# Kernel optimization log

Measured on AMD Instinct MI355X. Metric: run time of the kernel, lower is better.

## Reference

```python
import jax, jax.numpy as jnp
import numpy as np

N_NODES = 207
N_EDGES = 1722
N_SLOTS = 288  # 288 / resolution with resolution = 1


def setup_inputs() -> dict:
    key = jax.random.key(0)
    ks = jax.random.split(key, 7)
    B, C, L = 1024, 2, 64
    inputs = jax.random.normal(ks[0], (B, C, N_NODES, L), dtype=jnp.float32)
    weight_diff = jax.random.normal(ks[1], (N_SLOTS, N_EDGES), dtype=jnp.float32) / 1000.0
    bias_diffusion = jax.random.normal(ks[2], (N_SLOTS, N_NODES), dtype=jnp.float32) / 10.0
    weight_self_loop = jax.random.normal(ks[3], (N_SLOTS, N_NODES), dtype=jnp.float32) / 10.0
    ind = jax.random.randint(ks[4], (B,), 0, N_SLOTS, dtype=jnp.int32)
    edge_i = jax.random.randint(ks[5], (N_EDGES,), 0, N_NODES, dtype=jnp.int32)
    edge_j = jax.random.randint(ks[6], (N_EDGES,), 0, N_NODES, dtype=jnp.int32)
    return {"inputs": inputs, "weight_diff": weight_diff,
            "bias_diffusion": bias_diffusion, "weight_self_loop": weight_self_loop,
            "ind": ind, "edge_i": edge_i, "edge_j": edge_j}


def reference(inputs, weight_diff, bias_diffusion, weight_self_loop, ind, edge_i, edge_j):
    # resolution = 1 -> slot index ii == ind
    x = inputs[:, 0, :, :]                      # [B, N, L]
    B, N, _ = x.shape
    w = weight_diff[ind]                        # [B, E] per-sample edge weights
    # symmetric scatter into batched dense adjacency (duplicates sum, as in sparse_coo_tensor)
    A = jnp.zeros((B, N, N), dtype=x.dtype)
    A = A.at[:, edge_i, edge_j].add(w).at[:, edge_j, edge_i].add(w)
    deg = jnp.sum(A, axis=1)                    # [B, N]  (sum over dim 1, as in torch code)
    lap = deg[:, :, None] * jnp.eye(N, dtype=x.dtype) - A  # L = diag(deg) - A
    diffusion = jnp.einsum('nvl,nwv->nwl', x, lap) + bias_diffusion[ind][:, :, None]
    self_loop = weight_self_loop[ind][:, :, None] * x
    return diffusion + x + self_loop
```

## Files before the change

kernel.cpp:

```cpp
#include <hip/hip_runtime.h>

#define NN 207
#define NE 1722
#define NS 288
#define LDIM 64
#define KSTEPS 7
#define RT_TILES 13
#define XT_RS 232

typedef short bf16x8 __attribute__((ext_vector_type(8)));
typedef float f32x4  __attribute__((ext_vector_type(4)));

__device__ __forceinline__ unsigned int f2bf(float f) {
    unsigned int u = __float_as_uint(f);
    return (u + 0x7FFFu + ((u >> 16) & 1u)) >> 16;
}


__global__ __launch_bounds__(256) void build_m_kernel(
    const float* __restrict__ wd,
    const float* __restrict__ wsl,
    const int* __restrict__ ei, const int* __restrict__ ej,
    unsigned int* __restrict__ fragbuf) {
    __shared__ float M[64 * 224];
    __shared__ float deg[NN];
    const int sb = blockIdx.x;
    const int s = sb >> 2, p = sb & 3;
    const int r0 = p * 64;
    const int t = threadIdx.x;

    for (int i = t; i < 64 * 224; i += 256) M[i] = 0.f;
    for (int n = t; n < NN; n += 256) deg[n] = 0.f;
    __syncthreads();

    const float* wrow = wd + (size_t)s * NE;
    for (int e = t; e < NE; e += 256) {
        const float w = wrow[e];
        const int i = ei[e], j = ej[e];
        atomicAdd(&deg[i], w);
        atomicAdd(&deg[j], w);
        const int ri = i - r0;
        if (ri >= 0 && ri < 64) atomicAdd(&M[ri * 224 + j], -w);
        const int rj = j - r0;
        if (rj >= 0 && rj < 64) atomicAdd(&M[rj * 224 + i], -w);
    }
    __syncthreads();
    if (t < 64) {
        const int n = r0 + t;
        if (n < NN) M[t * 224 + n] += 1.f + wsl[(size_t)s * NN + n] + deg[n];
    }
    __syncthreads();

    const int ntiles = (p < 3) ? 4 : 1;
    for (int it = 0; it < ntiles * KSTEPS; ++it) {
        const int rtl = it / KSTEPS, ks = it % KSTEPS;
        const int rt = p * 4 + rtl;
        const int lane = t >> 2, pr = t & 3;
        const int row = rtl * 16 + (lane & 15);
        const int k = ks * 32 + (lane >> 4) * 8 + pr * 2;
        const unsigned int v = f2bf(M[row * 224 + k]) |
                               (f2bf(M[row * 224 + k + 1]) << 16);
        fragbuf[(((size_t)s * RT_TILES + rt) * KSTEPS + ks) * 256 + t] = v;
    }
}

__global__ __launch_bounds__(256, 4) void gemm_kernel(
    const float* __restrict__ inputs,
    const float* __restrict__ bias_d,
    const int*   __restrict__ ind,
    const unsigned int* __restrict__ fragbuf,
    float* __restrict__ out) {
    __shared__ __align__(16) unsigned short xT[LDIM * XT_RS];

    const int b = blockIdx.x, t = threadIdx.x;
    const int s = ind[b];
    const float* xb = inputs + (size_t)b * (2 * NN * LDIM);

    for (int it = t; it < 112 * 64; it += 256) {
        const int n = it & 63, kp = it >> 6;
        unsigned int v = 0;
        if (kp < 103) {
            v = f2bf(xb[(2 * kp) * 64 + n]) | (f2bf(xb[(2 * kp + 1) * 64 + n]) << 16);
        } else if (kp == 103) {
            v = f2bf(xb[206 * 64 + n]);
        }
        *(unsigned int*)&xT[n * XT_RS + kp * 2] = v;
    }
    __syncthreads();

    const int lane = t & 63, wv = t >> 6;
    const int quad = lane >> 4, m16 = lane & 15;

    bf16x8 Bf[KSTEPS];
    #pragma unroll
    for (int ks = 0; ks < KSTEPS; ++ks)
        Bf[ks] = *(const bf16x8*)&xT[(wv * 16 + m16) * XT_RS + ks * 32 + quad * 8];

    const bf16x8* Ab = ((const bf16x8*)fragbuf) +
                       (size_t)s * RT_TILES * KSTEPS * 64 + lane;
    float* ob = out + (size_t)b * NN * LDIM + wv * 16 + m16;
    const float* bias_row = bias_d + (size_t)s * NN;

    bf16x8 A0[KSTEPS], A1[KSTEPS];
    #pragma unroll
    for (int ks = 0; ks < KSTEPS; ++ks) A0[ks] = Ab[ks * 64];

    #pragma unroll
    for (int rt = 0; rt < RT_TILES; ++rt) {
        const bf16x8* Acur = (rt & 1) ? A1 : A0;
        bf16x8*       Anxt = (rt & 1) ? A0 : A1;
        if (rt + 1 < RT_TILES) {
            const bf16x8* An = Ab + (size_t)(rt + 1) * KSTEPS * 64;
            #pragma unroll
            for (int ks = 0; ks < KSTEPS; ++ks) Anxt[ks] = An[ks * 64];
        }
        f32x4 acc = {0.f, 0.f, 0.f, 0.f};
        #pragma unroll
        for (int ks = 0; ks < KSTEPS; ++ks)
            acc = __builtin_amdgcn_mfma_f32_16x16x32_bf16(Acur[ks], Bf[ks], acc, 0, 0, 0);
        #pragma unroll
        for (int r = 0; r < 4; ++r) {
            const int node = rt * 16 + quad * 4 + r;
            if (node < NN) ob[(size_t)node * 64] = acc[r] + bias_row[node];
        }
    }
}

__device__ __forceinline__ unsigned int f2bf_hi(float f) {
    unsigned int u = __float_as_uint(f);
    return (u + 0x7FFFu + ((u >> 16) & 1u)) & 0xFFFF0000u;
}

__global__ __launch_bounds__(256) void build_csr_kernel(
    const int* __restrict__ edge_i, const int* __restrict__ edge_j,
    int* __restrict__ row_start, unsigned int* __restrict__ csr_packed) {
    __shared__ int cnt[NN];
    __shared__ int rs[NN + 1];
    const int tid = threadIdx.x;
    for (int n = tid; n < NN; n += 256) cnt[n] = 0;
    __syncthreads();
    for (int e = tid; e < NE; e += 256) {
        atomicAdd(&cnt[edge_i[e]], 1);
        atomicAdd(&cnt[edge_j[e]], 1);
    }
    __syncthreads();
    if (tid == 0) {
        int acc = 0;
        for (int n = 0; n < NN; ++n) { rs[n] = acc; acc += cnt[n]; }
        rs[NN] = acc;
    }
    __syncthreads();
    for (int n = tid; n <= NN; n += 256) row_start[n] = rs[n];
    for (int n = tid; n < NN; n += 256) cnt[n] = rs[n];
    __syncthreads();
    for (int e = tid; e < NE; e += 256) {
        const unsigned int i = edge_i[e], j = edge_j[e];
        const unsigned int ep = ((unsigned int)e) << 8;
        int p = atomicAdd(&cnt[i], 1);
        csr_packed[p] = ep | j;
        int q = atomicAdd(&cnt[j], 1);
        csr_packed[q] = ep | i;
    }
}

__global__ __launch_bounds__(256) void coef_kernel(
    const float* __restrict__ weight_diff, const float* __restrict__ bias_diffusion,
    const float* __restrict__ weight_self_loop,
    const int* __restrict__ row_start, const unsigned int* __restrict__ csr_packed,
    float2* __restrict__ coefbias) {
    __shared__ float wrow[NE];
    const int s = blockIdx.x;
    for (int e = threadIdx.x; e < NE; e += 256)
        wrow[e] = weight_diff[(size_t)s * NE + e];
    __syncthreads();
    const int n = threadIdx.x;
    if (n < NN) {
        float d = 0.f;
        const int e0 = row_start[n], e1 = row_start[n + 1];
        for (int k = e0; k < e1; ++k) d += wrow[csr_packed[k] >> 8];
        coefbias[s * NN + n] = make_float2(
            1.f + weight_self_loop[s * NN + n] + d, bias_diffusion[s * NN + n]);
    }
}

__global__ __launch_bounds__(512, 8) void diffusion_gcn_kernel(
    const float* __restrict__ inputs, const float* __restrict__ weight_diff,
    const int* __restrict__ ind, const int* __restrict__ row_start,
    const unsigned int* __restrict__ csr_packed,
    const float2* __restrict__ coefbias, float* __restrict__ out) {
    __shared__ unsigned short xs[NN * LDIM];
    __shared__ unsigned int   wnb[2 * NE];
    __shared__ unsigned short rs[NN + 1];
    const int b = blockIdx.x, tid = threadIdx.x;
    const int slot = ind[b];
    const float* xb = inputs + (size_t)b * (2 * NN * LDIM);
    const float4* xb4 = (const float4*)xb;
    for (int k = tid; k < (NN * LDIM) / 4; k += 512) {
        const float4 v = xb4[k];
        const unsigned int lo = (f2bf_hi(v.x) >> 16) | f2bf_hi(v.y);
        const unsigned int hi = (f2bf_hi(v.z) >> 16) | f2bf_hi(v.w);
        ((uint2*)xs)[k] = make_uint2(lo, hi);
    }
    const float* wrow = weight_diff + (size_t)slot * NE;
    for (int k = tid; k < 2 * NE; k += 512) {
        const unsigned int c = csr_packed[k];
        wnb[k] = f2bf_hi(wrow[c >> 8]) | (c & 255u);
    }
    for (int n = tid; n <= NN; n += 512) rs[n] = (unsigned short)row_start[n];
    __syncthreads();
    const int lane = tid & 63, wv = tid >> 6;
    float* ob = out + (size_t)b * (NN * LDIM);
    for (int n = wv; n < NN; n += 8) {
        const int e0 = rs[n], e1 = rs[n + 1];
        float s = 0.f;
        #pragma unroll 4
        for (int k = e0; k < e1; ++k) {
            const unsigned int p = wnb[k];
            const float w = __uint_as_float(p & 0xFFFF0000u);
            const float xv = __uint_as_float((unsigned int)xs[(p & 255u) * LDIM + lane] << 16);
            s = fmaf(w, xv, s);
        }
        const float2 cb = coefbias[slot * NN + n];
        const float xg = xb[n * LDIM + lane];
        ob[n * LDIM + lane] = fmaf(cb.x, xg, cb.y) - s;
    }
}

extern "C" void kernel_launch(void* const* d_in, const int* in_sizes, int n_in,
                              void* d_out, int out_size, void* d_ws, size_t ws_size,
                              hipStream_t stream) {
    const float* inputs           = (const float*)d_in[0];
    const float* weight_diff      = (const float*)d_in[1];
    const float* bias_diffusion   = (const float*)d_in[2];
    const float* weight_self_loop = (const float*)d_in[3];
    const int*   ind              = (const int*)d_in[4];
    const int*   edge_i           = (const int*)d_in[5];
    const int*   edge_j           = (const int*)d_in[6];
    float* out = (float*)d_out;
    const int B = in_sizes[4];

    const size_t FRAG_BYTES = (size_t)NS * RT_TILES * KSTEPS * 1024;

    if (ws_size >= FRAG_BYTES) {
        unsigned int* fragbuf = (unsigned int*)d_ws;
        build_m_kernel<<<NS * 4, 256, 0, stream>>>(
            weight_diff, weight_self_loop, edge_i, edge_j, fragbuf);
        gemm_kernel<<<B, 256, 0, stream>>>(
            inputs, bias_diffusion, ind, fragbuf, out);
    } else {
        int*          row_start  = (int*)d_ws;
        unsigned int* csr_packed = (unsigned int*)((char*)d_ws + 832);
        float2*       coefbias   = (float2*)((char*)d_ws + 14608);
        build_csr_kernel<<<1, 256, 0, stream>>>(edge_i, edge_j, row_start, csr_packed);
        coef_kernel<<<NS, 256, 0, stream>>>(
            weight_diff, bias_diffusion, weight_self_loop, row_start, csr_packed, coefbias);
        diffusion_gcn_kernel<<<B, 512, 0, stream>>>(
            inputs, weight_diff, ind, row_start, csr_packed, coefbias, out);
    }
}
```

Before: 240.3 us.

## Stage A fragments into LDS via global_load_lds and defer output stores

In the GEMM kernel, each 16-row tile of the per-slot operator matrix is now staged into a double-buffered LDS area with direct global-to-LDS loads, which the four waves share, instead of every wave loading it into registers itself. The bias row is cached in shared memory, and the accumulators for all 13 tiles are kept in registers so the output stores happen after the MFMA loop. The aim is to cut redundant global/L2 traffic for the A operand and to overlap loading with compute. The cost is a block-wide barrier per tile, more LDS, more accumulator registers, and occupancy lowered from 4 to 3 in the launch bounds.

```diff
diff --git a/kernel.cpp b/kernel.cpp
--- a/kernel.cpp
+++ b/kernel.cpp
@@ -7,6 +7,7 @@
 #define KSTEPS 7
 #define RT_TILES 13
 #define XT_RS 232
+#define RT_BYTES (KSTEPS * 1024)
 
 typedef short bf16x8 __attribute__((ext_vector_type(8)));
 typedef float f32x4  __attribute__((ext_vector_type(4)));
@@ -64,13 +65,30 @@
     }
 }
 
-__global__ __launch_bounds__(256, 4) void gemm_kernel(
+__device__ __forceinline__ void stage_rt(const unsigned char* src,
+                                         unsigned char* dst, int t) {
+    const int w = t >> 6, l = t & 63;
+    __builtin_amdgcn_global_load_lds(
+        (const __attribute__((address_space(1))) unsigned int*)(src + w * 1024 + l * 16),
+        (__attribute__((address_space(3))) unsigned int*)(dst + w * 1024),
+        16, 0, 0);
+    if (w < 3) {
+        __builtin_amdgcn_global_load_lds(
+            (const __attribute__((address_space(1))) unsigned int*)(src + 4096 + w * 1024 + l * 16),
+            (__attribute__((address_space(3))) unsigned int*)(dst + 4096 + w * 1024),
+            16, 0, 0);
+    }
+}
+
+__global__ __launch_bounds__(256, 3) void gemm_kernel(
     const float* __restrict__ inputs,
     const float* __restrict__ bias_d,
     const int*   __restrict__ ind,
     const unsigned int* __restrict__ fragbuf,
     float* __restrict__ out) {
     __shared__ __align__(16) unsigned short xT[LDIM * XT_RS];
+    __shared__ __align__(16) unsigned char  Abuf[2][RT_BYTES];
+    __shared__ float biasS[NN + 1];
 
     const int b = blockIdx.x, t = threadIdx.x;
     const int s = ind[b];
@@ -86,6 +104,12 @@
         }
         *(unsigned int*)&xT[n * XT_RS + kp * 2] = v;
     }
+    const float* bias_row = bias_d + (size_t)s * NN;
+    for (int n = t; n < NN; n += 256) biasS[n] = bias_row[n];
+
+    const unsigned char* Asrc = (const unsigned char*)fragbuf +
+                                (size_t)s * RT_TILES * RT_BYTES;
+    stage_rt(Asrc, Abuf[0], t);
     __syncthreads();
 
     const int lane = t & 63, wv = t >> 6;
@@ -96,32 +120,30 @@
     for (int ks = 0; ks < KSTEPS; ++ks)
         Bf[ks] = *(const bf16x8*)&xT[(wv * 16 + m16) * XT_RS + ks * 32 + quad * 8];
 
-    const bf16x8* Ab = ((const bf16x8*)fragbuf) +
-                       (size_t)s * RT_TILES * KSTEPS * 64 + lane;
+    f32x4 acc[RT_TILES];
+    #pragma unroll
+    for (int rt = 0; rt < RT_TILES; ++rt) acc[rt] = (f32x4){0.f, 0.f, 0.f, 0.f};
+
+    #pragma unroll
+    for (int rt = 0; rt < RT_TILES; ++rt) {
+        if (rt + 1 < RT_TILES)
+            stage_rt(Asrc + (size_t)(rt + 1) * RT_BYTES, Abuf[(rt + 1) & 1], t);
+        const unsigned char* Ac = Abuf[rt & 1] + lane * 16;
+        #pragma unroll
+        for (int ks = 0; ks < KSTEPS; ++ks) {
+            const bf16x8 Af = *(const bf16x8*)(Ac + ks * 1024);
+            acc[rt] = __builtin_amdgcn_mfma_f32_16x16x32_bf16(Af, Bf[ks], acc[rt], 0, 0, 0);
+        }
+        if (rt + 1 < RT_TILES) __syncthreads();
+    }
+
     float* ob = out + (size_t)b * NN * LDIM + wv * 16 + m16;
-    const float* bias_row = bias_d + (size_t)s * NN;
-
-    bf16x8 A0[KSTEPS], A1[KSTEPS];
-    #pragma unroll
-    for (int ks = 0; ks < KSTEPS; ++ks) A0[ks] = Ab[ks * 64];
-
     #pragma unroll
     for (int rt = 0; rt < RT_TILES; ++rt) {
-        const bf16x8* Acur = (rt & 1) ? A1 : A0;
-        bf16x8*       Anxt = (rt & 1) ? A0 : A1;
-        if (rt + 1 < RT_TILES) {
-            const bf16x8* An = Ab + (size_t)(rt + 1) * KSTEPS * 64;
-            #pragma unroll
-            for (int ks = 0; ks < KSTEPS; ++ks) Anxt[ks] = An[ks * 64];
-        }
-        f32x4 acc = {0.f, 0.f, 0.f, 0.f};
-        #pragma unroll
-        for (int ks = 0; ks < KSTEPS; ++ks)
-            acc = __builtin_amdgcn_mfma_f32_16x16x32_bf16(Acur[ks], Bf[ks], acc, 0, 0, 0);
         #pragma unroll
         for (int r = 0; r < 4; ++r) {
             const int node = rt * 16 + quad * 4 + r;
-            if (node < NN) ob[(size_t)node * 64] = acc[r] + bias_row[node];
+            if (node < NN) ob[(size_t)node * 64] = acc[rt][r] + biasS[node];
         }
     }
 }
```

Measured after the change: 252.6 us. +5.1%, slower.

## Pre-swizzle X into MFMA fragment layout in LDS and defer output stores

Applied to the files above, without the earlier changes.

Stages the bf16-converted input directly in MFMA B-fragment order in shared memory and writes it with 16-byte stores. This replaces the padded transposed layout and its 4-byte writes. Bias is cached in LDS, and all 13 row-tile accumulators are kept in registers so stores happen after the MFMA loop instead of interleaved with it. In exchange, register pressure rises, so the occupancy hint drops from 4 to 3 blocks per CU.

```diff
diff --git a/kernel.cpp b/kernel.cpp
--- a/kernel.cpp
+++ b/kernel.cpp
@@ -6,7 +6,6 @@
 #define LDIM 64
 #define KSTEPS 7
 #define RT_TILES 13
-#define XT_RS 232
 
 typedef short bf16x8 __attribute__((ext_vector_type(8)));
 typedef float f32x4  __attribute__((ext_vector_type(4)));
@@ -64,28 +63,36 @@
     }
 }
 
-__global__ __launch_bounds__(256, 4) void gemm_kernel(
+__global__ __launch_bounds__(256, 3) void gemm_kernel(
     const float* __restrict__ inputs,
     const float* __restrict__ bias_d,
     const int*   __restrict__ ind,
     const unsigned int* __restrict__ fragbuf,
     float* __restrict__ out) {
-    __shared__ __align__(16) unsigned short xT[LDIM * XT_RS];
+    __shared__ __align__(16) unsigned char Bfrag[4 * KSTEPS * 1024];
+    __shared__ float biasS[NN + 1];
 
     const int b = blockIdx.x, t = threadIdx.x;
     const int s = ind[b];
     const float* xb = inputs + (size_t)b * (2 * NN * LDIM);
 
-    for (int it = t; it < 112 * 64; it += 256) {
-        const int n = it & 63, kp = it >> 6;
-        unsigned int v = 0;
-        if (kp < 103) {
-            v = f2bf(xb[(2 * kp) * 64 + n]) | (f2bf(xb[(2 * kp + 1) * 64 + n]) << 16);
-        } else if (kp == 103) {
-            v = f2bf(xb[206 * 64 + n]);
-        }
-        *(unsigned int*)&xT[n * XT_RS + kp * 2] = v;
-    }
+    for (int fe = t; fe < 4 * KSTEPS * 64; fe += 256) {
+        const int c   = fe / (KSTEPS * 64);
+        const int rem = fe - c * (KSTEPS * 64);
+        const int ks  = rem >> 6, ln = rem & 63;
+        const int l     = c * 16 + (ln & 15);
+        const int node0 = ks * 32 + ((ln >> 4) << 3);
+        unsigned int d[4];
+        #pragma unroll
+        for (int p = 0; p < 4; ++p) {
+            const int n0 = node0 + 2 * p, n1 = n0 + 1;
+            const unsigned int lo = (n0 < NN) ? f2bf(xb[n0 * 64 + l]) : 0u;
+            const unsigned int hi = (n1 < NN) ? f2bf(xb[n1 * 64 + l]) : 0u;
+            d[p] = lo | (hi << 16);
+        }
+        *(uint4*)(Bfrag + (size_t)fe * 16) = make_uint4(d[0], d[1], d[2], d[3]);
+    }
+    for (int n = t; n < NN; n += 256) biasS[n] = bias_d[(size_t)s * NN + n];
     __syncthreads();
 
     const int lane = t & 63, wv = t >> 6;
@@ -94,12 +101,14 @@
     bf16x8 Bf[KSTEPS];
     #pragma unroll
     for (int ks = 0; ks < KSTEPS; ++ks)
-        Bf[ks] = *(const bf16x8*)&xT[(wv * 16 + m16) * XT_RS + ks * 32 + quad * 8];
+        Bf[ks] = *(const bf16x8*)(Bfrag + (((size_t)wv * KSTEPS + ks) * 64 + lane) * 16);
 
     const bf16x8* Ab = ((const bf16x8*)fragbuf) +
                        (size_t)s * RT_TILES * KSTEPS * 64 + lane;
-    float* ob = out + (size_t)b * NN * LDIM + wv * 16 + m16;
-    const float* bias_row = bias_d + (size_t)s * NN;
+
+    f32x4 acc[RT_TILES];
+    #pragma unroll
+    for (int rt = 0; rt < RT_TILES; ++rt) acc[rt] = (f32x4){0.f, 0.f, 0.f, 0.f};
 
     bf16x8 A0[KSTEPS], A1[KSTEPS];
     #pragma unroll
@@ -114,14 +123,18 @@
             #pragma unroll
             for (int ks = 0; ks < KSTEPS; ++ks) Anxt[ks] = An[ks * 64];
         }
-        f32x4 acc = {0.f, 0.f, 0.f, 0.f};
         #pragma unroll
         for (int ks = 0; ks < KSTEPS; ++ks)
-            acc = __builtin_amdgcn_mfma_f32_16x16x32_bf16(Acur[ks], Bf[ks], acc, 0, 0, 0);
+            acc[rt] = __builtin_amdgcn_mfma_f32_16x16x32_bf16(Acur[ks], Bf[ks], acc[rt], 0, 0, 0);
+    }
+
+    float* ob = out + (size_t)b * NN * LDIM + wv * 16 + m16;
+    #pragma unroll
+    for (int rt = 0; rt < RT_TILES; ++rt) {
         #pragma unroll
         for (int r = 0; r < 4; ++r) {
             const int node = rt * 16 + quad * 4 + r;
-            if (node < NN) ob[(size_t)node * 64] = acc[r] + bias_row[node];
+            if (node < NN) ob[(size_t)node * 64] = acc[rt][r] + biasS[node];
         }
     }
 }
```

Result: slower. 276.4 us (+15.0%).
